# Kernel tuning notes

Measured on AMD Instinct MI355X. Metric: run time of the kernel, lower is better.

## Reference

```python
import jax, jax.numpy as jnp
import numpy as np
import math

# Static config (matches init_kwargs): C4 rotation group, 14x14 grid
B = 2
CIN = 96
MID = 96
HEADS = 8
COUT = 96
G = 4            # group elements (0/90/180/270 deg rotations)
S = 14           # spatial size == max_pos_embedding
HID = 16         # hidden width of the row/col embedding MLP (Conv2d 1->16)
DPOS = MID // 3                  # 32: row / col embedding dims
DG = MID - 2 * DPOS              # 32: group embedding dim


def setup_inputs() -> dict:
    key = jax.random.key(0)
    ks = jax.random.split(key, 12)

    def lin(k, shape, scale):
        return jax.random.normal(k, shape, jnp.float32) * scale

    x = jax.random.normal(ks[0], (B, CIN, G, S, S), jnp.float32)
    # 1x1x1 Conv3d weights == per-position linear layers [out, in]
    Wq = lin(ks[1], (MID * HEADS, CIN), 1.0 / np.sqrt(CIN)); bq = jnp.zeros((MID * HEADS,), jnp.float32)
    Wk = lin(ks[2], (MID * HEADS, CIN), 1.0 / np.sqrt(CIN)); bk = jnp.zeros((MID * HEADS,), jnp.float32)
    Wv = lin(ks[3], (MID * HEADS, CIN), 1.0 / np.sqrt(CIN)); bv = jnp.zeros((MID * HEADS,), jnp.float32)
    Wo = lin(ks[4], (COUT, MID * HEADS), 1.0 / np.sqrt(MID * HEADS)); bo = jnp.zeros((COUT,), jnp.float32)
    # row embedding MLP: scalar -> 16 -> LayerNorm -> Swish -> DPOS
    rw1 = lin(ks[5], (HID,), 1.0); rb1 = jnp.zeros((HID,), jnp.float32)
    rgam = jnp.ones((HID,), jnp.float32); rbet = jnp.zeros((HID,), jnp.float32)
    rw2 = lin(ks[6], (HID, DPOS), 1.0 / np.sqrt(HID)); rb2 = jnp.zeros((DPOS,), jnp.float32)
    # col embedding MLP
    cw1 = lin(ks[7], (HID,), 1.0); cb1 = jnp.zeros((HID,), jnp.float32)
    cgam = jnp.ones((HID,), jnp.float32); cbet = jnp.zeros((HID,), jnp.float32)
    cw2 = lin(ks[8], (HID, DPOS), 1.0 / np.sqrt(HID)); cb2 = jnp.zeros((DPOS,), jnp.float32)
    # group element embedding table
    gemb = lin(ks[9], (G, DG), 0.02)

    # Relative-position buffers: rel coordinate (k-i)/(S-1) in [-1,1], rotated by
    # each group element (left action of the rotation on R^2).  [G, S, S, S, S]
    d = (jnp.arange(S)[None, :] - jnp.arange(S)[:, None]).astype(jnp.float32) / (S - 1)
    dr = jnp.broadcast_to(d[:, None, :, None], (S, S, S, S))   # row offset (k-i)
    dc = jnp.broadcast_to(d[None, :, None, :], (S, S, S, S))   # col offset (l-j)
    ang = jnp.arange(G, dtype=jnp.float32) * (np.pi / 2.0)
    cs = jnp.cos(ang)[:, None, None, None, None]
    sn = jnp.sin(ang)[:, None, None, None, None]
    row_rel = cs * dr - sn * dc
    col_rel = sn * dr + cs * dc
    # relative group-element indices acted on by each group element v: [G, G, G]
    gi = jnp.arange(G)
    g_idx = (gi[None, None, :] - gi[None, :, None] + gi[:, None, None]) % G

    return {"x": x, "Wq": Wq, "bq": bq, "Wk": Wk, "bk": bk, "Wv": Wv, "bv": bv,
            "Wo": Wo, "bo": bo,
            "rw1": rw1, "rb1": rb1, "rgam": rgam, "rbet": rbet, "rw2": rw2, "rb2": rb2,
            "cw1": cw1, "cb1": cb1, "cgam": cgam, "cbet": cbet, "cw2": cw2, "cb2": cb2,
            "gemb": gemb, "row_rel": row_rel, "col_rel": col_rel, "g_idx": g_idx}


def _embed(rel, w1, b1, gam, bet, w2, b2):
    # Conv2d(1->16, k=1) + channel LayerNorm + Swish + Conv2d(16->DPOS, k=1)
    h = rel[..., None] * w1 + b1                                   # [..., 16]
    mu = jnp.mean(h, axis=-1, keepdims=True)
    var = jnp.var(h, axis=-1, keepdims=True)
    h = (h - mu) / jnp.sqrt(var + 1e-5) * gam + bet
    h = h * jax.nn.sigmoid(h)                                      # Swish
    return h @ w2 + b2                                             # [..., DPOS]


def reference(x, Wq, bq, Wk, bk, Wv, bv, Wo, bo,
              rw1, rb1, rgam, rbet, rw2, rb2,
              cw1, cb1, cgam, cbet, cw2, cb2,
              gemb, row_rel, col_rel, g_idx):
    b = x.shape[0]

    def proj(W, bias):
        y = jnp.einsum('bcgij,dc->bdgij', x, W) + bias[None, :, None, None, None]
        return y.reshape(b, MID, HEADS, G, S, S)   # split channels as (mid, heads)

    q = proj(Wq, bq)
    k = proj(Wk, bk)
    v = proj(Wv, bv)

    q_row = q[:, :DPOS]
    q_col = q[:, DPOS:2 * DPOS]
    q_grp = q[:, 2 * DPOS:]

    row_e = _embed(row_rel, rw1, rb1, rgam, rbet, rw2, rb2)        # [G,S,S,S,S,DPOS]
    col_e = _embed(col_rel, cw1, cb1, cgam, cbet, cw2, cb2)

    row_s = jnp.einsum('bchgij,vijklc->bhvgijkl', q_row, row_e)
    col_s = jnp.einsum('bchgij,vijklc->bhvgijkl', q_col, col_e)
    g_s = jnp.einsum('bchgij,vgmc->bhvgijm', q_grp, gemb[g_idx])
    content = jnp.einsum('bchgij,bchmkl->bhgijmkl', q, k)

    # broadcast add into [b, h, v, g, i, j, m, k, l]
    scores = (jnp.expand_dims(row_s + col_s, -3)
              + g_s[..., None, None]
              + content[:, :, None]) / math.sqrt(CIN)

    sh = scores.shape
    probs = jax.nn.softmax(scores.reshape(sh[:-3] + (-1,)), axis=-1).reshape(sh)

    vo = jnp.einsum('bhvgijmkl,bchmkl->bchvij', probs, v)
    vo = vo.reshape(b, MID * HEADS, G, S, S)
    return jnp.einsum('bcgij,dc->bdgij', vo, Wo) + bo[None, :, None, None, None]
```

## Files before the change

kernel.cpp:

```cpp
#include <hip/hip_runtime.h>
#include <hip/hip_bf16.h>

constexpr int kB   = 2;
constexpr int kH   = 8;
constexpr int kG   = 4;
constexpr int kS   = 14;
constexpr int kSS  = 196;
constexpr int kKey = 784;
constexpr int kKeyP = 800;
constexpr int kMid = 96;
constexpr int kQR  = 28;
constexpr int kPS  = 808;
constexpr int kTS  = 36;
constexpr int kXS  = 104;
constexpr float kScl = 0.10206207261596577f;
constexpr float kK2  = 0.14724663682f;
constexpr float kCc  = 11.5415603272f;

typedef __attribute__((ext_vector_type(8))) short bf16x8;
typedef __attribute__((ext_vector_type(4))) float f32x4;

constexpr size_t SZ_QKb = (size_t)kB*kH*kG*kSS*kMid/2;
constexpr size_t OFF_Qb = 0;
constexpr size_t OFF_Kb = OFF_Qb + SZ_QKb;
constexpr size_t OFF_V  = OFF_Kb + SZ_QKb;
constexpr size_t SZ_V   = (size_t)kB*kH*kMid*kKeyP/2;
constexpr size_t OFF_FR = OFF_V + SZ_V;
constexpr size_t OFF_FC = OFF_FR + 27*32;
constexpr size_t OFF_WOH = OFF_FC + 27*32;

__global__ __launch_bounds__(512, 8)
void k_qkv(const float* __restrict__ x,
           const float* __restrict__ Wq, const float* __restrict__ bq,
           const float* __restrict__ Wk, const float* __restrict__ bk,
           const float* __restrict__ Wv, const float* __restrict__ bv,
           __hip_bfloat16* __restrict__ Qb, __hip_bfloat16* __restrict__ Kb,
           __hip_bfloat16* __restrict__ Vb,
           const float* __restrict__ rw1, const float* __restrict__ rb1,
           const float* __restrict__ rgam, const float* __restrict__ rbet,
           const float* __restrict__ rw2, const float* __restrict__ rb2,
           const float* __restrict__ cw1, const float* __restrict__ cb1,
           const float* __restrict__ cgam, const float* __restrict__ cbet,
           const float* __restrict__ cw2, const float* __restrict__ cb2,
           float* __restrict__ frow, float* __restrict__ fcol,
           const float* __restrict__ Wo, __hip_bfloat16* __restrict__ Woh,
           float* __restrict__ out0) {
  const int bid = blockIdx.x;
  const int ten = blockIdx.y;
  const int tid = threadIdx.x;
  const int nq = bid % 4;
  const int mc = (bid / 4) % 6;
  const int g  = (bid / 24) % 4;
  const int b  = bid / 96;
  const int d0 = mc * 128;
  const int ij0 = nq * 49;
  const float* W    = (ten == 0) ? Wq : (ten == 1) ? Wk : Wv;
  const float* bias = (ten == 0) ? bq : (ten == 1) ? bk : bv;

  {
    int zidx = (ten*192 + bid)*512 + tid;
    if (zidx < 37632) ((float4*)out0)[zidx] = make_float4(0.f, 0.f, 0.f, 0.f);
  }

  __shared__ alignas(16) __hip_bfloat16 Xt[64][kXS];
  __shared__ alignas(16) __hip_bfloat16 Ws[128][kXS];

  for (int idx = tid; idx < 24*64; idx += 512) {
    int cq = idx >> 6, r = idx & 63;
    float4 v = make_float4(0.f, 0.f, 0.f, 0.f);
    if (r < 49) {
      const float* xp = x + (((size_t)b*96 + cq*4)*4 + (size_t)g)*196 + ij0 + r;
      v.x = xp[0]; v.y = xp[784]; v.z = xp[1568]; v.w = xp[2352];
    }
    ushort4 u;
    u.x = __bfloat16_as_ushort(__float2bfloat16(v.x));
    u.y = __bfloat16_as_ushort(__float2bfloat16(v.y));
    u.z = __bfloat16_as_ushort(__float2bfloat16(v.z));
    u.w = __bfloat16_as_ushort(__float2bfloat16(v.w));
    *(ushort4*)(&Xt[r][cq*4]) = u;
  }
  for (int idx = tid; idx < 128*24; idx += 512) {
    int dl = idx / 24, cq = idx - dl*24;
    float4 v = *(const float4*)(W + (size_t)(d0 + dl)*96 + cq*4);
    ushort4 u;
    u.x = __bfloat16_as_ushort(__float2bfloat16(v.x));
    u.y = __bfloat16_as_ushort(__float2bfloat16(v.y));
    u.z = __bfloat16_as_ushort(__float2bfloat16(v.z));
    u.w = __bfloat16_as_ushort(__float2bfloat16(v.w));
    *(ushort4*)(&Ws[dl][cq*4]) = u;
  }
  __syncthreads();

  {
    const int lane = tid & 63;
    const int wave = tid >> 6;
    const int col  = lane & 15;
    const int quad = lane >> 4;
    const short* ar = (const short*)(&Ws[wave*16 + col][0]);
    bf16x8 a0 = *(const bf16x8*)(ar + 0*32 + quad*8);
    bf16x8 a1 = *(const bf16x8*)(ar + 1*32 + quad*8);
    bf16x8 a2 = *(const bf16x8*)(ar + 2*32 + quad*8);
    float4 b4 = *(const float4*)(bias + d0 + wave*16 + quad*4);
    float bb[4] = {b4.x, b4.y, b4.z, b4.w};

#pragma unroll
    for (int nt = 0; nt < 4; ++nt) {
      const short* xr = (const short*)(&Xt[nt*16 + col][0]);
      bf16x8 x0 = *(const bf16x8*)(xr + 0*32 + quad*8);
      bf16x8 x1 = *(const bf16x8*)(xr + 1*32 + quad*8);
      bf16x8 x2 = *(const bf16x8*)(xr + 2*32 + quad*8);
      f32x4 acc = {0.f, 0.f, 0.f, 0.f};
      acc = __builtin_amdgcn_mfma_f32_16x16x32_bf16(a0, x0, acc, 0, 0, 0);
      acc = __builtin_amdgcn_mfma_f32_16x16x32_bf16(a1, x1, acc, 0, 0, 0);
      acc = __builtin_amdgcn_mfma_f32_16x16x32_bf16(a2, x2, acc, 0, 0, 0);
      int rl = nt*16 + col;
      if (rl < 49) {
        int ij = ij0 + rl;
#pragma unroll
        for (int r = 0; r < 4; ++r) {
          int d = d0 + wave*16 + quad*4 + r;
          int c = d >> 3, h = d & 7;
          float val = acc[r] + bb[r];
          if (ten == 2) {
            Vb[((size_t)((b*8 + h)*96 + c))*kKeyP + ij*4 + g] = __float2bfloat16(val);
          } else {
            __hip_bfloat16* dst = (ten == 0) ? Qb : Kb;
            dst[((size_t)((b*8 + h)*4 + g)*196 + ij)*96 + c] = __float2bfloat16(val);
          }
        }
      }
    }
  }

  if (ten == 1) {
    for (int idx = bid*512 + tid; idx < 73728; idx += 192*512) {
      int h = idx / 9216, rem = idx - h*9216;
      int d = rem / 96, c = rem - d*96;
      Woh[idx] = __float2bfloat16(Wo[(size_t)d*768 + c*8 + h]);
    }
  }
  if (ten == 2 && bid < 16) {
    for (int idx = tid; idx < 96*16; idx += 512) {
      int c = idx >> 4, kp = idx & 15;
      Vb[((size_t)(bid*96 + c))*kKeyP + kKey + kp] = __float2bfloat16(0.f);
    }
  }
  if (ten == 0 && bid == 0 && tid < 54) {
    int t = tid;
    int which = t / 27;
    int n = t % 27;
    float tv = (float)(n - 13) / 13.0f;
    const float* w1  = which ? cw1  : rw1;
    const float* b1  = which ? cb1  : rb1;
    const float* gam = which ? cgam : rgam;
    const float* bet = which ? cbet : rbet;
    const float* w2  = which ? cw2  : rw2;
    const float* b2  = which ? cb2  : rb2;
    float h[16];
    float mu = 0.f;
#pragma unroll
    for (int d = 0; d < 16; ++d) { h[d] = tv * w1[d] + b1[d]; mu += h[d]; }
    mu *= (1.0f/16.0f);
    float var = 0.f;
#pragma unroll
    for (int d = 0; d < 16; ++d) { float z = h[d] - mu; var += z*z; }
    var *= (1.0f/16.0f);
    float rstd = rsqrtf(var + 1e-5f);
#pragma unroll
    for (int d = 0; d < 16; ++d) {
      float z = (h[d] - mu) * rstd * gam[d] + bet[d];
      h[d] = z / (1.0f + expf(-z));
    }
    float* outp = (which ? fcol : frow) + n*32;
    for (int c = 0; c < 32; ++c) {
      float o = b2[c];
#pragma unroll
      for (int d = 0; d < 16; ++d) o += h[d] * w2[d*32 + c];
      outp[c] = o;
    }
  }
}

__global__ __launch_bounds__(512, 4)
void k_attn(const __hip_bfloat16* __restrict__ Qb, const __hip_bfloat16* __restrict__ Kb,
            const float* __restrict__ frow_g, const float* __restrict__ fcol_g,
            const float* __restrict__ gemb_g,
            const __hip_bfloat16* __restrict__ Vb,
            const __hip_bfloat16* __restrict__ Woh,
            const float* __restrict__ bo, float* __restrict__ out) {
  const int tid = threadIdx.x;
  const int bid = blockIdx.x;
  const int xcd  = bid & 7;
  const int slot = bid >> 3;
  const int sub  = (slot >= 28);
  const int within = slot - sub*28;
  const int bh = xcd*2 + sub;
  const int qi = within >> 1;
  const int jhalf = within & 1;

  __shared__ alignas(16) char poolA[19104];
  __shared__ alignas(16) __hip_bfloat16 contl[kQR][kPS];
  __shared__ alignas(16) float ArrE[kQR][28];
  __shared__ alignas(16) float AclE[kQR][28];
  __shared__ alignas(16) float AgEall[4][kQR][4];
  __shared__ float T[4][kQR][14];
  __shared__ float DinvS[4][kQR];

  float (*qs)[96] = (float(*)[96])poolA;
  float* frowS = (float*)(poolA + 10752);
  float* fcolS = (float*)(poolA + 10752 + 3888);
  float* gembS = (float*)(poolA + 10752 + 2*3888);
  __hip_bfloat16 (*vos)[104] = (__hip_bfloat16(*)[104])poolA;

  const short* Qs = (const short*)Qb;
  const short* Ks = (const short*)Kb;

  for (int idx = tid; idx < kQR*96; idx += 512) {
    int q = idx / 96, c = idx - q*96;
    int g = q / 7, jq = q - g*7;
    qs[q][c] = __bfloat162float(
        Qb[((size_t)((bh*4 + g)*kSS + qi*14 + jhalf*7 + jq))*96 + c]);
  }
  for (int idx = tid; idx < 864; idx += 512) {
    int s = idx >> 5, c = idx & 31;
    frowS[s*kTS + c] = frow_g[idx] * kK2;
    fcolS[s*kTS + c] = fcol_g[idx] * kK2;
  }
  if (tid < 128) gembS[(tid >> 5)*kTS + (tid & 31)] = gemb_g[tid] * kK2;
  __syncthreads();

  for (int idx = tid; idx < kQR*24; idx += 512) {
    int r = idx / 24, c2 = idx - r*24;
    contl[r][784 + c2] = __float2bfloat16(0.f);
  }
  {
    const int lane = tid & 63;
    const int wave = tid >> 6;
    const int col  = lane & 15;
    const int quad = lane >> 4;

    bf16x8 afrag[2][3];
#pragma unroll
    for (int mt = 0; mt < 2; ++mt) {
      int m = mt*16 + col;
      int q = (m < kQR) ? m : 0;
      const short* qrow = Qs +
          ((size_t)((bh*4 + q/7)*kSS + qi*14 + jhalf*7 + q%7))*96;
#pragma unroll
      for (int ks = 0; ks < 3; ++ks)
        afrag[mt][ks] = *(const bf16x8*)(qrow + ks*32 + quad*8);
    }

    for (int nt = wave; nt < 49; nt += 8) {
      int kl = nt*16 + col;
      const short* krow = Ks + ((size_t)(bh*kKey + kl))*96;
      bf16x8 b0 = *(const bf16x8*)(krow + 0*32 + quad*8);
      bf16x8 b1 = *(const bf16x8*)(krow + 1*32 + quad*8);
      bf16x8 b2 = *(const bf16x8*)(krow + 2*32 + quad*8);
      f32x4 c0 = {0.f,0.f,0.f,0.f};
      f32x4 c1 = {0.f,0.f,0.f,0.f};
      c0 = __builtin_amdgcn_mfma_f32_16x16x32_bf16(afrag[0][0], b0, c0, 0, 0, 0);
      c0 = __builtin_amdgcn_mfma_f32_16x16x32_bf16(afrag[0][1], b1, c0, 0, 0, 0);
      c0 = __builtin_amdgcn_mfma_f32_16x16x32_bf16(afrag[0][2], b2, c0, 0, 0, 0);
      c1 = __builtin_amdgcn_mfma_f32_16x16x32_bf16(afrag[1][0], b0, c1, 0, 0, 0);
      c1 = __builtin_amdgcn_mfma_f32_16x16x32_bf16(afrag[1][1], b1, c1, 0, 0, 0);
      c1 = __builtin_amdgcn_mfma_f32_16x16x32_bf16(afrag[1][2], b2, c1, 0, 0, 0);
      int ijn = kl % 196, mk = kl / 196;
#pragma unroll
      for (int r = 0; r < 4; ++r) {
        int q0 = quad*4 + r;
        contl[q0][ijn*4 + mk] = __float2bfloat16(exp2f(c0[r]*kK2 - kCc));
        int q1 = 16 + quad*4 + r;
        if (q1 < kQR)
          contl[q1][ijn*4 + mk] = __float2bfloat16(exp2f(c1[r]*kK2 - kCc));
      }
    }
  }

  for (int t = tid; t < kQR*58; t += 512) {
    int q = t / 58, s = t - q*58;
    float acc = 0.f;
    if (s < 27) {
#pragma unroll
      for (int c = 0; c < 32; ++c) acc += qs[q][c] * frowS[s*kTS + c];
      ArrE[q][s] = exp2f(acc);
    } else if (s < 54) {
      int n = s - 27;
#pragma unroll
      for (int c = 0; c < 32; ++c) acc += qs[q][32+c] * fcolS[n*kTS + c];
      AclE[q][n] = exp2f(acc);
    } else {
      int p = s - 54;
#pragma unroll
      for (int c = 0; c < 32; ++c) acc += qs[q][64+c] * gembS[p*kTS + c];
      float e = exp2f(acc);
      int gq = q / 7;
#pragma unroll
      for (int vv = 0; vv < 4; ++vv)
        AgEall[vv][q][(p + gq - vv + 8) & 3] = e;
    }
  }
  __syncthreads();

  const int actv = (tid < 392);
  const int qB  = actv ? (tid / 14) : 0;
  const int kkB = actv ? (tid % 14) : 0;
  const int jlB = jhalf*7 + (qB % 7);
  const int daB = kkB - qi;
  const int half = actv ? (tid / 196) : 0;
  const int ijC  = actv ? (tid % 196) : 0;
  const int kkC = ijC / 14;
  const int llC = ijC % 14;
  const int daC = kkC - qi;

  if (actv) {
    f32x4 ag0 = *(const f32x4*)(&AgEall[0][qB][0]);
    f32x4 ag1 = *(const f32x4*)(&AgEall[1][qB][0]);
    f32x4 ag2 = *(const f32x4*)(&AgEall[2][qB][0]);
    f32x4 ag3 = *(const f32x4*)(&AgEall[3][qB][0]);
    const float* Ar = &ArrE[qB][13];
    const float* Ac = &AclE[qB][13];
    float a0 = 0.f, a1 = 0.f, a2 = 0.f, a3 = 0.f;
#pragma unroll
    for (int ll = 0; ll < 14; ++ll) {
      const int db = ll - jlB;
      ushort4 u = *(const ushort4*)(&contl[qB][(kkB*14 + ll)*4]);
      float e0 = __uint_as_float((unsigned)u.x << 16);
      float e1 = __uint_as_float((unsigned)u.y << 16);
      float e2 = __uint_as_float((unsigned)u.z << 16);
      float e3 = __uint_as_float((unsigned)u.w << 16);
      a0 += Ac[ db] * (e0*ag0.x + e1*ag0.y + e2*ag0.z + e3*ag0.w);
      a1 += Ar[-db] * (e0*ag1.x + e1*ag1.y + e2*ag1.z + e3*ag1.w);
      a2 += Ac[-db] * (e0*ag2.x + e1*ag2.y + e2*ag2.z + e3*ag2.w);
      a3 += Ar[ db] * (e0*ag3.x + e1*ag3.y + e2*ag3.z + e3*ag3.w);
    }
    T[0][qB][kkB] = Ar[ daB] * a0;
    T[1][qB][kkB] = Ac[ daB] * a1;
    T[2][qB][kkB] = Ar[-daB] * a2;
    T[3][qB][kkB] = Ac[-daB] * a3;
  }
  __syncthreads();
  if (tid < 112) {
    int v = tid / 28, q = tid - v*28;
    float dsum = 0.f;
#pragma unroll
    for (int kk = 0; kk < 14; ++kk) dsum += T[v][q][kk];
    DinvS[v][q] = 1.0f / dsum;
  }
  __syncthreads();

  if (actv) {
    unsigned p32[kQR];
#pragma unroll
    for (int q = 0; q < kQR; ++q)
      p32[q] = *(const unsigned*)(&contl[q][ijC*4 + half*2]);
#pragma unroll
    for (int v = 0; v < 4; ++v) {
      const int s1a = (v==0) ? 1 : (v==2) ? -1 : 0;
      const int s1b = (v==1) ? -1 : (v==3) ? 1 : 0;
      const int s2a = (v==1) ? 1 : (v==3) ? -1 : 0;
      const int s2b = (v==0) ? 1 : (v==2) ? -1 : 0;
#pragma unroll
      for (int jq = 0; jq < 7; ++jq) {
        const int db = llC - (jhalf*7 + jq);
        const int ai = s1a*daC + s1b*db, ci = s2a*daC + s2b*db;
        float am0 = 0.f, am1 = 0.f;
#pragma unroll
        for (int gq = 0; gq < 4; ++gq) {
          const int q = gq*7 + jq;
          const float fq = ArrE[q][13 + ai] * AclE[q][13 + ci] * DinvS[v][q];
          unsigned u = p32[q];
          float e0 = __uint_as_float(u << 16);
          float e1 = __uint_as_float(u & 0xffff0000u);
          am0 += e0 * (AgEall[v][q][half*2]     * fq);
          am1 += e1 * (AgEall[v][q][half*2 + 1] * fq);
        }
        __hip_bfloat16* pp = &contl[jq*4 + v][ijC*4 + half*2];
        pp[0] = __float2bfloat16(am0);
        pp[1] = __float2bfloat16(am1);
      }
    }
  }
  __syncthreads();

  const int lane = tid & 63;
  const int wave = tid >> 6;
  const int col  = lane & 15;
  const int quad = lane >> 4;
  const int b_ = bh >> 3, h_ = bh & 7;

  {
    const short* Bp = (const short*)Vb + ((size_t)bh*96)*kKeyP + quad*8;
#pragma unroll
    for (int tk = 0; tk < 2; ++tk) {
      int t = wave + tk*8;
      if (t < 12) {
        int mt = t / 6, nt = t - mt*6;
        int crow = nt*16 + col;
        int prow = mt*16 + col; if (prow >= kQR) prow = 0;
        const short* ap = (const short*)(&contl[prow][0]) + quad*8;
        const short* bp = Bp + (size_t)crow*kKeyP;
        f32x4 acc = {0.f,0.f,0.f,0.f};
        for (int ks = 0; ks < 25; ++ks) {
          bf16x8 a = *(const bf16x8*)(ap + ks*32);
          bf16x8 b = *(const bf16x8*)(bp + ks*32);
          acc = __builtin_amdgcn_mfma_f32_16x16x32_bf16(a, b, acc, 0, 0, 0);
        }
#pragma unroll
        for (int r = 0; r < 4; ++r)
          vos[mt*16 + quad*4 + r][crow] = __float2bfloat16(acc[r]);
      }
    }
  }
  __syncthreads();

  {
    const short* wb = (const short*)Woh + (size_t)h_*9216;
#pragma unroll
    for (int tk = 0; tk < 2; ++tk) {
      int t = wave + tk*8;
      if (t < 12) {
        int mt = t / 6, dt = t - mt*6;
        f32x4 acc = {0.f,0.f,0.f,0.f};
#pragma unroll
        for (int ks = 0; ks < 3; ++ks) {
          bf16x8 a = *(const bf16x8*)(&vos[mt*16 + col][ks*32 + quad*8]);
          bf16x8 b = *(const bf16x8*)(wb + (size_t)(dt*16 + col)*96 + ks*32 + quad*8);
          acc = __builtin_amdgcn_mfma_f32_16x16x32_bf16(a, b, acc, 0, 0, 0);
        }
        const int d = dt*16 + col;
        const float bias = (h_ == 0) ? bo[d] : 0.f;
#pragma unroll
        for (int r = 0; r < 4; ++r) {
          int rr = mt*16 + quad*4 + r;
          if (rr < kQR) {
            int jq = rr >> 2, vv = rr & 3;
            int ijq = qi*14 + jhalf*7 + jq;
            atomicAdd(&out[((size_t)(b_*96 + d)*4 + vv)*kSS + ijq], acc[r] + bias);
          }
        }
      }
    }
  }
}

extern "C" void kernel_launch(void* const* d_in, const int* in_sizes, int n_in,
                              void* d_out, int out_size, void* d_ws, size_t ws_size,
                              hipStream_t stream) {
  const float* x    = (const float*)d_in[0];
  const float* Wq   = (const float*)d_in[1];
  const float* bq   = (const float*)d_in[2];
  const float* Wk   = (const float*)d_in[3];
  const float* bk   = (const float*)d_in[4];
  const float* Wv   = (const float*)d_in[5];
  const float* bv   = (const float*)d_in[6];
  const float* Wo   = (const float*)d_in[7];
  const float* bo   = (const float*)d_in[8];
  const float* rw1  = (const float*)d_in[9];
  const float* rb1  = (const float*)d_in[10];
  const float* rgam = (const float*)d_in[11];
  const float* rbet = (const float*)d_in[12];
  const float* rw2  = (const float*)d_in[13];
  const float* rb2  = (const float*)d_in[14];
  const float* cw1  = (const float*)d_in[15];
  const float* cb1  = (const float*)d_in[16];
  const float* cgam = (const float*)d_in[17];
  const float* cbet = (const float*)d_in[18];
  const float* cw2  = (const float*)d_in[19];
  const float* cb2  = (const float*)d_in[20];
  const float* gemb = (const float*)d_in[21];

  float* ws = (float*)d_ws;
  __hip_bfloat16* Qb = (__hip_bfloat16*)(ws + OFF_Qb);
  __hip_bfloat16* Kb = (__hip_bfloat16*)(ws + OFF_Kb);
  __hip_bfloat16* Vb = (__hip_bfloat16*)(ws + OFF_V);
  float* Frow = ws + OFF_FR;
  float* Fcol = ws + OFF_FC;
  __hip_bfloat16* Woh = (__hip_bfloat16*)(ws + OFF_WOH);
  float* out  = (float*)d_out;

  k_qkv<<<dim3(192, 3), 512, 0, stream>>>(x, Wq, bq, Wk, bk, Wv, bv, Qb, Kb, Vb,
                                          rw1, rb1, rgam, rbet, rw2, rb2,
                                          cw1, cb1, cgam, cbet, cw2, cb2,
                                          Frow, Fcol, Wo, Woh, out);
  k_attn<<<448, 512, 0, stream>>>(Qb, Kb, Frow, Fcol, gemb, Vb, Woh, bo, out);
}
```

Baseline: 163.1 us.

## Split attention query tiles into quarter-rows to double block count

The attention kernel now processes 12-16 query rows per block (a quarter of a spatial row across 4 group elements) instead of 28, doubling the grid from 448 to 896 blocks. The per-block MFMA tiles shrink to a single 16-row tile, and the shared-memory footprint is reduced so that launch bounds can request 6 blocks per CU. The intent is better occupancy and load balance across CUs. In exchange, each block re-reads the full K and V panels for fewer queries, so global/L2 traffic rises and MFMA tiles are partly wasted (12 of 16 rows for JN=3), and atomic adds are spread over more blocks.

Result: slower. 170.7 us (+4.6%).

```diff
diff --git a/kernel.cpp b/kernel.cpp
--- a/kernel.cpp
+++ b/kernel.cpp
@@ -9,7 +9,6 @@
 constexpr int kKey = 784;
 constexpr int kKeyP = 800;
 constexpr int kMid = 96;
-constexpr int kQR  = 28;
 constexpr int kPS  = 808;
 constexpr int kTS  = 36;
 constexpr int kXS  = 104;
@@ -19,6 +18,8 @@
 
 typedef __attribute__((ext_vector_type(8))) short bf16x8;
 typedef __attribute__((ext_vector_type(4))) float f32x4;
+
+template<int N> struct IC { static constexpr int value = N; };
 
 constexpr size_t SZ_QKb = (size_t)kB*kH*kG*kSS*kMid/2;
 constexpr size_t OFF_Qb = 0;
@@ -181,7 +182,7 @@
   }
 }
 
-__global__ __launch_bounds__(512, 4)
+__global__ __launch_bounds__(512, 6)
 void k_attn(const __hip_bfloat16* __restrict__ Qb, const __hip_bfloat16* __restrict__ Kb,
             const float* __restrict__ frow_g, const float* __restrict__ fcol_g,
             const float* __restrict__ gemb_g,
@@ -192,34 +193,37 @@
   const int bid = blockIdx.x;
   const int xcd  = bid & 7;
   const int slot = bid >> 3;
-  const int sub  = (slot >= 28);
-  const int within = slot - sub*28;
+  const int sub  = (slot >= 56);
+  const int within = slot - sub*56;
   const int bh = xcd*2 + sub;
-  const int qi = within >> 1;
-  const int jhalf = within & 1;
-
-  __shared__ alignas(16) char poolA[19104];
-  __shared__ alignas(16) __hip_bfloat16 contl[kQR][kPS];
-  __shared__ alignas(16) float ArrE[kQR][28];
-  __shared__ alignas(16) float AclE[kQR][28];
-  __shared__ alignas(16) float AgEall[4][kQR][4];
-  __shared__ float T[4][kQR][14];
-  __shared__ float DinvS[4][kQR];
+  const int qi = within >> 2;
+  const int jsel = within & 3;
+  const int JN = (jsel & 1) ? 3 : 4;
+  const int jbase = (jsel==0) ? 0 : (jsel==1) ? 4 : (jsel==2) ? 7 : 11;
+  const int NQ = 4*JN;
+
+  __shared__ alignas(16) char poolA[14496];
+  __shared__ alignas(16) __hip_bfloat16 contl[16][kPS];
+  __shared__ alignas(16) float ArrE[16][28];
+  __shared__ alignas(16) float AclE[16][28];
+  __shared__ alignas(16) float AgEall[4][16][4];
+  __shared__ float T[4][16][14];
+  __shared__ float DinvS[4][16];
 
   float (*qs)[96] = (float(*)[96])poolA;
-  float* frowS = (float*)(poolA + 10752);
-  float* fcolS = (float*)(poolA + 10752 + 3888);
-  float* gembS = (float*)(poolA + 10752 + 2*3888);
+  float* frowS = (float*)(poolA + 6144);
+  float* fcolS = (float*)(poolA + 6144 + 3888);
+  float* gembS = (float*)(poolA + 6144 + 2*3888);
   __hip_bfloat16 (*vos)[104] = (__hip_bfloat16(*)[104])poolA;
 
   const short* Qs = (const short*)Qb;
   const short* Ks = (const short*)Kb;
 
-  for (int idx = tid; idx < kQR*96; idx += 512) {
+  for (int idx = tid; idx < NQ*96; idx += 512) {
     int q = idx / 96, c = idx - q*96;
-    int g = q / 7, jq = q - g*7;
+    int g = q / JN, jq = q - g*JN;
     qs[q][c] = __bfloat162float(
-        Qb[((size_t)((bh*4 + g)*kSS + qi*14 + jhalf*7 + jq))*96 + c]);
+        Qb[((size_t)((bh*4 + g)*kSS + qi*14 + jbase + jq))*96 + c]);
   }
   for (int idx = tid; idx < 864; idx += 512) {
     int s = idx >> 5, c = idx & 31;
@@ -229,7 +233,7 @@
   if (tid < 128) gembS[(tid >> 5)*kTS + (tid & 31)] = gemb_g[tid] * kK2;
   __syncthreads();
 
-  for (int idx = tid; idx < kQR*24; idx += 512) {
+  for (int idx = tid; idx < 16*24; idx += 512) {
     int r = idx / 24, c2 = idx - r*24;
     contl[r][784 + c2] = __float2bfloat16(0.f);
   }
@@ -239,16 +243,15 @@
     const int col  = lane & 15;
     const int quad = lane >> 4;
 
-    bf16x8 afrag[2][3];
-#pragma unroll
-    for (int mt = 0; mt < 2; ++mt) {
-      int m = mt*16 + col;
-      int q = (m < kQR) ? m : 0;
+    bf16x8 afrag[3];
+    {
+      int q = (col < NQ) ? col : 0;
+      int g = q / JN, jq = q - g*JN;
       const short* qrow = Qs +
-          ((size_t)((bh*4 + q/7)*kSS + qi*14 + jhalf*7 + q%7))*96;
+          ((size_t)((bh*4 + g)*kSS + qi*14 + jbase + jq))*96;
 #pragma unroll
       for (int ks = 0; ks < 3; ++ks)
-        afrag[mt][ks] = *(const bf16x8*)(qrow + ks*32 + quad*8);
+        afrag[ks] = *(const bf16x8*)(qrow + ks*32 + quad*8);
     }
 
     for (int nt = wave; nt < 49; nt += 8) {
@@ -258,26 +261,20 @@
       bf16x8 b1 = *(const bf16x8*)(krow + 1*32 + quad*8);
       bf16x8 b2 = *(const bf16x8*)(krow + 2*32 + quad*8);
       f32x4 c0 = {0.f,0.f,0.f,0.f};
-      f32x4 c1 = {0.f,0.f,0.f,0.f};
-      c0 = __builtin_amdgcn_mfma_f32_16x16x32_bf16(afrag[0][0], b0, c0, 0, 0, 0);
-      c0 = __builtin_amdgcn_mfma_f32_16x16x32_bf16(afrag[0][1], b1, c0, 0, 0, 0);
-      c0 = __builtin_amdgcn_mfma_f32_16x16x32_bf16(afrag[0][2], b2, c0, 0, 0, 0);
-      c1 = __builtin_amdgcn_mfma_f32_16x16x32_bf16(afrag[1][0], b0, c1, 0, 0, 0);
-      c1 = __builtin_amdgcn_mfma_f32_16x16x32_bf16(afrag[1][1], b1, c1, 0, 0, 0);
-      c1 = __builtin_amdgcn_mfma_f32_16x16x32_bf16(afrag[1][2], b2, c1, 0, 0, 0);
+      c0 = __builtin_amdgcn_mfma_f32_16x16x32_bf16(afrag[0], b0, c0, 0, 0, 0);
+      c0 = __builtin_amdgcn_mfma_f32_16x16x32_bf16(afrag[1], b1, c0, 0, 0, 0);
+      c0 = __builtin_amdgcn_mfma_f32_16x16x32_bf16(afrag[2], b2, c0, 0, 0, 0);
       int ijn = kl % 196, mk = kl / 196;
 #pragma unroll
       for (int r = 0; r < 4; ++r) {
         int q0 = quad*4 + r;
-        contl[q0][ijn*4 + mk] = __float2bfloat16(exp2f(c0[r]*kK2 - kCc));
-        int q1 = 16 + quad*4 + r;
-        if (q1 < kQR)
-          contl[q1][ijn*4 + mk] = __float2bfloat16(exp2f(c1[r]*kK2 - kCc));
+        if (q0 < NQ)
+          contl[q0][ijn*4 + mk] = __float2bfloat16(exp2f(c0[r]*kK2 - kCc));
       }
     }
   }
 
-  for (int t = tid; t < kQR*58; t += 512) {
+  for (int t = tid; t < NQ*58; t += 512) {
     int q = t / 58, s = t - q*58;
     float acc = 0.f;
     if (s < 27) {
@@ -294,7 +291,7 @@
 #pragma unroll
       for (int c = 0; c < 32; ++c) acc += qs[q][64+c] * gembS[p*kTS + c];
       float e = exp2f(acc);
-      int gq = q / 7;
+      int gq = q / JN;
 #pragma unroll
       for (int vv = 0; vv < 4; ++vv)
         AgEall[vv][q][(p + gq - vv + 8) & 3] = e;
@@ -302,18 +299,19 @@
   }
   __syncthreads();
 
+  const int actvB = (tid < NQ*14);
+  const int qB  = actvB ? (tid / 14) : 0;
+  const int kkB = actvB ? (tid % 14) : 0;
+  const int jlB = jbase + (qB % JN);
+  const int daB = kkB - qi;
   const int actv = (tid < 392);
-  const int qB  = actv ? (tid / 14) : 0;
-  const int kkB = actv ? (tid % 14) : 0;
-  const int jlB = jhalf*7 + (qB % 7);
-  const int daB = kkB - qi;
   const int half = actv ? (tid / 196) : 0;
   const int ijC  = actv ? (tid % 196) : 0;
   const int kkC = ijC / 14;
   const int llC = ijC % 14;
   const int daC = kkC - qi;
 
-  if (actv) {
+  if (actvB) {
     f32x4 ag0 = *(const f32x4*)(&AgEall[0][qB][0]);
     f32x4 ag1 = *(const f32x4*)(&AgEall[1][qB][0]);
     f32x4 ag2 = *(const f32x4*)(&AgEall[2][qB][0]);
@@ -340,47 +338,54 @@
     T[3][qB][kkB] = Ac[-daB] * a3;
   }
   __syncthreads();
-  if (tid < 112) {
-    int v = tid / 28, q = tid - v*28;
-    float dsum = 0.f;
-#pragma unroll
-    for (int kk = 0; kk < 14; ++kk) dsum += T[v][q][kk];
-    DinvS[v][q] = 1.0f / dsum;
-  }
-  __syncthreads();
-
-  if (actv) {
-    unsigned p32[kQR];
-#pragma unroll
-    for (int q = 0; q < kQR; ++q)
-      p32[q] = *(const unsigned*)(&contl[q][ijC*4 + half*2]);
-#pragma unroll
-    for (int v = 0; v < 4; ++v) {
-      const int s1a = (v==0) ? 1 : (v==2) ? -1 : 0;
-      const int s1b = (v==1) ? -1 : (v==3) ? 1 : 0;
-      const int s2a = (v==1) ? 1 : (v==3) ? -1 : 0;
-      const int s2b = (v==0) ? 1 : (v==2) ? -1 : 0;
-#pragma unroll
-      for (int jq = 0; jq < 7; ++jq) {
-        const int db = llC - (jhalf*7 + jq);
-        const int ai = s1a*daC + s1b*db, ci = s2a*daC + s2b*db;
-        float am0 = 0.f, am1 = 0.f;
-#pragma unroll
-        for (int gq = 0; gq < 4; ++gq) {
-          const int q = gq*7 + jq;
-          const float fq = ArrE[q][13 + ai] * AclE[q][13 + ci] * DinvS[v][q];
-          unsigned u = p32[q];
-          float e0 = __uint_as_float(u << 16);
-          float e1 = __uint_as_float(u & 0xffff0000u);
-          am0 += e0 * (AgEall[v][q][half*2]     * fq);
-          am1 += e1 * (AgEall[v][q][half*2 + 1] * fq);
+  if (tid < 64) {
+    int v = tid >> 4, q = tid & 15;
+    if (q < NQ) {
+      float dsum = 0.f;
+#pragma unroll
+      for (int kk = 0; kk < 14; ++kk) dsum += T[v][q][kk];
+      DinvS[v][q] = 1.0f / dsum;
+    }
+  }
+  __syncthreads();
+
+  auto passC = [&](auto jn) {
+    constexpr int JNv = decltype(jn)::value;
+    constexpr int NQv = 4*JNv;
+    if (actv) {
+      unsigned p32[NQv];
+#pragma unroll
+      for (int q = 0; q < NQv; ++q)
+        p32[q] = *(const unsigned*)(&contl[q][ijC*4 + half*2]);
+#pragma unroll
+      for (int v = 0; v < 4; ++v) {
+        const int s1a = (v==0) ? 1 : (v==2) ? -1 : 0;
+        const int s1b = (v==1) ? -1 : (v==3) ? 1 : 0;
+        const int s2a = (v==1) ? 1 : (v==3) ? -1 : 0;
+        const int s2b = (v==0) ? 1 : (v==2) ? -1 : 0;
+#pragma unroll
+        for (int jq = 0; jq < JNv; ++jq) {
+          const int db = llC - (jbase + jq);
+          const int ai = s1a*daC + s1b*db, ci = s2a*daC + s2b*db;
+          float am0 = 0.f, am1 = 0.f;
+#pragma unroll
+          for (int gq = 0; gq < 4; ++gq) {
+            const int q = gq*JNv + jq;
+            const float fq = ArrE[q][13 + ai] * AclE[q][13 + ci] * DinvS[v][q];
+            unsigned u = p32[q];
+            float e0 = __uint_as_float(u << 16);
+            float e1 = __uint_as_float(u & 0xffff0000u);
+            am0 += e0 * (AgEall[v][q][half*2]     * fq);
+            am1 += e1 * (AgEall[v][q][half*2 + 1] * fq);
+          }
+          __hip_bfloat16* pp = &contl[jq*4 + v][ijC*4 + half*2];
+          pp[0] = __float2bfloat16(am0);
+          pp[1] = __float2bfloat16(am1);
         }
-        __hip_bfloat16* pp = &contl[jq*4 + v][ijC*4 + half*2];
-        pp[0] = __float2bfloat16(am0);
-        pp[1] = __float2bfloat16(am1);
       }
     }
-  }
+  };
+  if (JN == 4) passC(IC<4>{}); else passC(IC<3>{});
   __syncthreads();
 
   const int lane = tid & 63;
@@ -389,56 +394,42 @@
   const int quad = lane >> 4;
   const int b_ = bh >> 3, h_ = bh & 7;
 
-  {
-    const short* Bp = (const short*)Vb + ((size_t)bh*96)*kKeyP + quad*8;
-#pragma unroll
-    for (int tk = 0; tk < 2; ++tk) {
-      int t = wave + tk*8;
-      if (t < 12) {
-        int mt = t / 6, nt = t - mt*6;
-        int crow = nt*16 + col;
-        int prow = mt*16 + col; if (prow >= kQR) prow = 0;
-        const short* ap = (const short*)(&contl[prow][0]) + quad*8;
-        const short* bp = Bp + (size_t)crow*kKeyP;
-        f32x4 acc = {0.f,0.f,0.f,0.f};
-        for (int ks = 0; ks < 25; ++ks) {
-          bf16x8 a = *(const bf16x8*)(ap + ks*32);
-          bf16x8 b = *(const bf16x8*)(bp + ks*32);
-          acc = __builtin_amdgcn_mfma_f32_16x16x32_bf16(a, b, acc, 0, 0, 0);
-        }
-#pragma unroll
-        for (int r = 0; r < 4; ++r)
-          vos[mt*16 + quad*4 + r][crow] = __float2bfloat16(acc[r]);
-      }
-    }
-  }
-  __syncthreads();
-
-  {
+  if (wave < 6) {
+    const int crow = wave*16 + col;
+    const int prow = (col < NQ) ? col : 0;
+    const short* ap = (const short*)(&contl[prow][0]) + quad*8;
+    const short* bp = (const short*)Vb + ((size_t)bh*96 + crow)*kKeyP + quad*8;
+    f32x4 acc = {0.f,0.f,0.f,0.f};
+    for (int ks = 0; ks < 25; ++ks) {
+      bf16x8 a = *(const bf16x8*)(ap + ks*32);
+      bf16x8 b = *(const bf16x8*)(bp + ks*32);
+      acc = __builtin_amdgcn_mfma_f32_16x16x32_bf16(a, b, acc, 0, 0, 0);
+    }
+#pragma unroll
+    for (int r = 0; r < 4; ++r)
+      vos[quad*4 + r][crow] = __float2bfloat16(acc[r]);
+  }
+  __syncthreads();
+
+  if (wave < 6) {
     const short* wb = (const short*)Woh + (size_t)h_*9216;
-#pragma unroll
-    for (int tk = 0; tk < 2; ++tk) {
-      int t = wave + tk*8;
-      if (t < 12) {
-        int mt = t / 6, dt = t - mt*6;
-        f32x4 acc = {0.f,0.f,0.f,0.f};
-#pragma unroll
-        for (int ks = 0; ks < 3; ++ks) {
-          bf16x8 a = *(const bf16x8*)(&vos[mt*16 + col][ks*32 + quad*8]);
-          bf16x8 b = *(const bf16x8*)(wb + (size_t)(dt*16 + col)*96 + ks*32 + quad*8);
-          acc = __builtin_amdgcn_mfma_f32_16x16x32_bf16(a, b, acc, 0, 0, 0);
-        }
-        const int d = dt*16 + col;
-        const float bias = (h_ == 0) ? bo[d] : 0.f;
-#pragma unroll
-        for (int r = 0; r < 4; ++r) {
-          int rr = mt*16 + quad*4 + r;
-          if (rr < kQR) {
-            int jq = rr >> 2, vv = rr & 3;
-            int ijq = qi*14 + jhalf*7 + jq;
-            atomicAdd(&out[((size_t)(b_*96 + d)*4 + vv)*kSS + ijq], acc[r] + bias);
-          }
-        }
+    const int dt = wave;
+    f32x4 acc = {0.f,0.f,0.f,0.f};
+#pragma unroll
+    for (int ks = 0; ks < 3; ++ks) {
+      bf16x8 a = *(const bf16x8*)(&vos[col][ks*32 + quad*8]);
+      bf16x8 b = *(const bf16x8*)(wb + (size_t)(dt*16 + col)*96 + ks*32 + quad*8);
+      acc = __builtin_amdgcn_mfma_f32_16x16x32_bf16(a, b, acc, 0, 0, 0);
+    }
+    const int d = dt*16 + col;
+    const float bias = (h_ == 0) ? bo[d] : 0.f;
+#pragma unroll
+    for (int r = 0; r < 4; ++r) {
+      int rr = quad*4 + r;
+      if (rr < NQ) {
+        int jq = rr >> 2, vv = rr & 3;
+        int ijq = qi*14 + jbase + jq;
+        atomicAdd(&out[((size_t)(b_*96 + d)*4 + vv)*kSS + ijq], acc[r] + bias);
       }
     }
   }
@@ -483,5 +474,5 @@
                                           rw1, rb1, rgam, rbet, rw2, rb2,
                                           cw1, cb1, cgam, cbet, cw2, cb2,
                                           Frow, Fcol, Wo, Woh, out);
-  k_attn<<<448, 512, 0, stream>>>(Qb, Kb, Frow, Fcol, gemb, Vb, Woh, bo, out);
+  k_attn<<<896, 512, 0, stream>>>(Qb, Kb, Frow, Fcol, gemb, Vb, Woh, bo, out);
 }
```

## Shrink attention LDS footprint and fuse denominator reduction via shuffles

Applied to the files above, without the earlier changes.

Removes the staged fp32 copies of Q and the row/col/group embedding tables from shared memory, computing the positional dot products directly from global bf16 Q and fp32 tables. The per-query denominator partial sums are reduced with 16-lane xor shuffles instead of a shared T array plus an extra barrier pass. Contiguous-row padding drops from 808 to 800, and launch bounds are raised to 6 blocks per CU to exploit the smaller LDS. The risks are more global/L2 traffic in the embedding stage, possible LDS bank conflicts without padding, and register pressure under the tighter bound.

After: 209.2 us. 1.28x slower.

```diff
diff --git a/kernel.cpp b/kernel.cpp
--- a/kernel.cpp
+++ b/kernel.cpp
@@ -10,8 +10,7 @@
 constexpr int kKeyP = 800;
 constexpr int kMid = 96;
 constexpr int kQR  = 28;
-constexpr int kPS  = 808;
-constexpr int kTS  = 36;
+constexpr int kPS  = 800;
 constexpr int kXS  = 104;
 constexpr float kScl = 0.10206207261596577f;
 constexpr float kK2  = 0.14724663682f;
@@ -19,6 +18,10 @@
 
 typedef __attribute__((ext_vector_type(8))) short bf16x8;
 typedef __attribute__((ext_vector_type(4))) float f32x4;
+
+__device__ __forceinline__ float b2f(short s) {
+  return __uint_as_float(((unsigned)(unsigned short)s) << 16);
+}
 
 constexpr size_t SZ_QKb = (size_t)kB*kH*kG*kSS*kMid/2;
 constexpr size_t OFF_Qb = 0;
@@ -181,7 +184,7 @@
   }
 }
 
-__global__ __launch_bounds__(512, 4)
+__global__ __launch_bounds__(512, 6)
 void k_attn(const __hip_bfloat16* __restrict__ Qb, const __hip_bfloat16* __restrict__ Kb,
             const float* __restrict__ frow_g, const float* __restrict__ fcol_g,
             const float* __restrict__ gemb_g,
@@ -198,41 +201,20 @@
   const int qi = within >> 1;
   const int jhalf = within & 1;
 
-  __shared__ alignas(16) char poolA[19104];
   __shared__ alignas(16) __hip_bfloat16 contl[kQR][kPS];
-  __shared__ alignas(16) float ArrE[kQR][28];
-  __shared__ alignas(16) float AclE[kQR][28];
-  __shared__ alignas(16) float AgEall[4][kQR][4];
-  __shared__ float T[4][kQR][14];
-  __shared__ float DinvS[4][kQR];
-
-  float (*qs)[96] = (float(*)[96])poolA;
-  float* frowS = (float*)(poolA + 10752);
-  float* fcolS = (float*)(poolA + 10752 + 3888);
-  float* gembS = (float*)(poolA + 10752 + 2*3888);
-  __hip_bfloat16 (*vos)[104] = (__hip_bfloat16(*)[104])poolA;
+  __shared__ alignas(16) char pool2[8512];
+
+  float (*ArrE)[28]    = (float(*)[28])pool2;
+  float (*AclE)[28]    = (float(*)[28])(pool2 + 3136);
+  float (*AgEall)[kQR][4] = (float(*)[kQR][4])(pool2 + 6272);
+  float* DinvS2        = (float*)(pool2 + 8064);
+  __hip_bfloat16 (*vos)[104] = (__hip_bfloat16(*)[104])pool2;
 
   const short* Qs = (const short*)Qb;
   const short* Ks = (const short*)Kb;
 
-  for (int idx = tid; idx < kQR*96; idx += 512) {
-    int q = idx / 96, c = idx - q*96;
-    int g = q / 7, jq = q - g*7;
-    qs[q][c] = __bfloat162float(
-        Qb[((size_t)((bh*4 + g)*kSS + qi*14 + jhalf*7 + jq))*96 + c]);
-  }
-  for (int idx = tid; idx < 864; idx += 512) {
-    int s = idx >> 5, c = idx & 31;
-    frowS[s*kTS + c] = frow_g[idx] * kK2;
-    fcolS[s*kTS + c] = fcol_g[idx] * kK2;
-  }
-  if (tid < 128) gembS[(tid >> 5)*kTS + (tid & 31)] = gemb_g[tid] * kK2;
-  __syncthreads();
-
-  for (int idx = tid; idx < kQR*24; idx += 512) {
-    int r = idx / 24, c2 = idx - r*24;
-    contl[r][784 + c2] = __float2bfloat16(0.f);
-  }
+  if (tid < 448) { int r = tid >> 4, kp = tid & 15; contl[r][784 + kp] = __float2bfloat16(0.f); }
+
   {
     const int lane = tid & 63;
     const int wave = tid >> 6;
@@ -277,36 +259,88 @@
     }
   }
 
-  for (int t = tid; t < kQR*58; t += 512) {
-    int q = t / 58, s = t - q*58;
-    float acc = 0.f;
-    if (s < 27) {
-#pragma unroll
-      for (int c = 0; c < 32; ++c) acc += qs[q][c] * frowS[s*kTS + c];
-      ArrE[q][s] = exp2f(acc);
-    } else if (s < 54) {
-      int n = s - 27;
-#pragma unroll
-      for (int c = 0; c < 32; ++c) acc += qs[q][32+c] * fcolS[n*kTS + c];
-      AclE[q][n] = exp2f(acc);
-    } else {
-      int p = s - 54;
-#pragma unroll
-      for (int c = 0; c < 32; ++c) acc += qs[q][64+c] * gembS[p*kTS + c];
-      float e = exp2f(acc);
-      int gq = q / 7;
-#pragma unroll
-      for (int vv = 0; vv < 4; ++vv)
-        AgEall[vv][q][(p + gq - vv + 8) & 3] = e;
+  {
+    auto dot32 = [](const short* qp, const float* tp) -> float {
+      float acc = 0.f;
+#pragma unroll
+      for (int k8 = 0; k8 < 4; ++k8) {
+        bf16x8 qv = *(const bf16x8*)(qp + k8*8);
+        float4 ta = *(const float4*)(tp + k8*8);
+        float4 tb = *(const float4*)(tp + k8*8 + 4);
+        acc += b2f(qv[0])*ta.x + b2f(qv[1])*ta.y + b2f(qv[2])*ta.z + b2f(qv[3])*ta.w;
+        acc += b2f(qv[4])*tb.x + b2f(qv[5])*tb.y + b2f(qv[6])*tb.z + b2f(qv[7])*tb.w;
+      }
+      return acc;
+    };
+    for (int t = tid; t < kQR*58; t += 512) {
+      int q = t / 58, s = t - q*58;
+      const short* qp = Qs +
+          ((size_t)((bh*4 + q/7)*kSS + qi*14 + jhalf*7 + q%7))*96;
+      if (s < 27) {
+        ArrE[q][s] = exp2f(dot32(qp, frow_g + s*32) * kK2);
+      } else if (s < 54) {
+        AclE[q][s-27] = exp2f(dot32(qp + 32, fcol_g + (s-27)*32) * kK2);
+      } else {
+        int p = s - 54;
+        float e = exp2f(dot32(qp + 64, gemb_g + p*32) * kK2);
+        int gq = q / 7;
+#pragma unroll
+        for (int vv = 0; vv < 4; ++vv)
+          AgEall[vv][q][(p + gq - vv + 8) & 3] = e;
+      }
     }
   }
   __syncthreads();
 
+  if (tid < 448) {
+    const int qB  = tid >> 4;
+    const int kkB = tid & 15;
+    float t0 = 0.f, t1 = 0.f, t2 = 0.f, t3 = 0.f;
+    if (kkB < 14) {
+      const int jlB = jhalf*7 + (qB % 7);
+      const int daB = kkB - qi;
+      f32x4 ag0 = *(const f32x4*)(&AgEall[0][qB][0]);
+      f32x4 ag1 = *(const f32x4*)(&AgEall[1][qB][0]);
+      f32x4 ag2 = *(const f32x4*)(&AgEall[2][qB][0]);
+      f32x4 ag3 = *(const f32x4*)(&AgEall[3][qB][0]);
+      const float* Ar = &ArrE[qB][13];
+      const float* Ac = &AclE[qB][13];
+      float a0 = 0.f, a1 = 0.f, a2 = 0.f, a3 = 0.f;
+#pragma unroll
+      for (int ll = 0; ll < 14; ++ll) {
+        const int db = ll - jlB;
+        ushort4 u = *(const ushort4*)(&contl[qB][(kkB*14 + ll)*4]);
+        float e0 = __uint_as_float((unsigned)u.x << 16);
+        float e1 = __uint_as_float((unsigned)u.y << 16);
+        float e2 = __uint_as_float((unsigned)u.z << 16);
+        float e3 = __uint_as_float((unsigned)u.w << 16);
+        a0 += Ac[ db] * (e0*ag0.x + e1*ag0.y + e2*ag0.z + e3*ag0.w);
+        a1 += Ar[-db] * (e0*ag1.x + e1*ag1.y + e2*ag1.z + e3*ag1.w);
+        a2 += Ac[-db] * (e0*ag2.x + e1*ag2.y + e2*ag2.z + e3*ag2.w);
+        a3 += Ar[ db] * (e0*ag3.x + e1*ag3.y + e2*ag3.z + e3*ag3.w);
+      }
+      t0 = Ar[ daB] * a0;
+      t1 = Ac[ daB] * a1;
+      t2 = Ar[-daB] * a2;
+      t3 = Ac[-daB] * a3;
+    }
+#pragma unroll
+    for (int off = 1; off < 16; off <<= 1) {
+      t0 += __shfl_xor(t0, off, 16);
+      t1 += __shfl_xor(t1, off, 16);
+      t2 += __shfl_xor(t2, off, 16);
+      t3 += __shfl_xor(t3, off, 16);
+    }
+    if (kkB == 0) {
+      DinvS2[0*28 + qB] = 1.0f / t0;
+      DinvS2[1*28 + qB] = 1.0f / t1;
+      DinvS2[2*28 + qB] = 1.0f / t2;
+      DinvS2[3*28 + qB] = 1.0f / t3;
+    }
+  }
+  __syncthreads();
+
   const int actv = (tid < 392);
-  const int qB  = actv ? (tid / 14) : 0;
-  const int kkB = actv ? (tid % 14) : 0;
-  const int jlB = jhalf*7 + (qB % 7);
-  const int daB = kkB - qi;
   const int half = actv ? (tid / 196) : 0;
   const int ijC  = actv ? (tid % 196) : 0;
   const int kkC = ijC / 14;
@@ -314,42 +348,6 @@
   const int daC = kkC - qi;
 
   if (actv) {
-    f32x4 ag0 = *(const f32x4*)(&AgEall[0][qB][0]);
-    f32x4 ag1 = *(const f32x4*)(&AgEall[1][qB][0]);
-    f32x4 ag2 = *(const f32x4*)(&AgEall[2][qB][0]);
-    f32x4 ag3 = *(const f32x4*)(&AgEall[3][qB][0]);
-    const float* Ar = &ArrE[qB][13];
-    const float* Ac = &AclE[qB][13];
-    float a0 = 0.f, a1 = 0.f, a2 = 0.f, a3 = 0.f;
-#pragma unroll
-    for (int ll = 0; ll < 14; ++ll) {
-      const int db = ll - jlB;
-      ushort4 u = *(const ushort4*)(&contl[qB][(kkB*14 + ll)*4]);
-      float e0 = __uint_as_float((unsigned)u.x << 16);
-      float e1 = __uint_as_float((unsigned)u.y << 16);
-      float e2 = __uint_as_float((unsigned)u.z << 16);
-      float e3 = __uint_as_float((unsigned)u.w << 16);
-      a0 += Ac[ db] * (e0*ag0.x + e1*ag0.y + e2*ag0.z + e3*ag0.w);
-      a1 += Ar[-db] * (e0*ag1.x + e1*ag1.y + e2*ag1.z + e3*ag1.w);
-      a2 += Ac[-db] * (e0*ag2.x + e1*ag2.y + e2*ag2.z + e3*ag2.w);
-      a3 += Ar[ db] * (e0*ag3.x + e1*ag3.y + e2*ag3.z + e3*ag3.w);
-    }
-    T[0][qB][kkB] = Ar[ daB] * a0;
-    T[1][qB][kkB] = Ac[ daB] * a1;
-    T[2][qB][kkB] = Ar[-daB] * a2;
-    T[3][qB][kkB] = Ac[-daB] * a3;
-  }
-  __syncthreads();
-  if (tid < 112) {
-    int v = tid / 28, q = tid - v*28;
-    float dsum = 0.f;
-#pragma unroll
-    for (int kk = 0; kk < 14; ++kk) dsum += T[v][q][kk];
-    DinvS[v][q] = 1.0f / dsum;
-  }
-  __syncthreads();
-
-  if (actv) {
     unsigned p32[kQR];
 #pragma unroll
     for (int q = 0; q < kQR; ++q)
@@ -368,7 +366,7 @@
 #pragma unroll
         for (int gq = 0; gq < 4; ++gq) {
           const int q = gq*7 + jq;
-          const float fq = ArrE[q][13 + ai] * AclE[q][13 + ci] * DinvS[v][q];
+          const float fq = ArrE[q][13 + ai] * AclE[q][13 + ci] * DinvS2[v*28 + q];
           unsigned u = p32[q];
           float e0 = __uint_as_float(u << 16);
           float e1 = __uint_as_float(u & 0xffff0000u);
```
